# Kernel tuning notes

Hardware: AMD Instinct MI355X
Metric: run time of the kernel (lower is better)

Reference implementation:

```python
import jax, jax.numpy as jnp
import numpy as np

DIM = 256

def _feat(x):
    # ELU(x) + 1 feature map (positive features for linear attention)
    return jax.nn.elu(x) + 1.0

def setup_inputs() -> dict:
    key = jax.random.key(0)
    ks = jax.random.split(key, 9)
    B, L, D = 8, 4096, DIM
    s = 1.0 / np.sqrt(D)
    return {
        'q': jax.random.normal(ks[0], (B, L, D), jnp.float32),
        'k': jax.random.normal(ks[1], (B, L, D), jnp.float32),
        'v': jax.random.normal(ks[2], (B, L, D), jnp.float32),
        'Wq': jax.random.normal(ks[3], (D, D), jnp.float32) * s,
        'bq': jnp.zeros((D,), jnp.float32),
        'Wk': jax.random.normal(ks[4], (D, D), jnp.float32) * s,
        'bk': jnp.zeros((D,), jnp.float32),
        'Wv': jax.random.normal(ks[5], (D, D), jnp.float32) * s,
        'bv': jnp.zeros((D,), jnp.float32),
    }

def reference(q, k, v, Wq, bq, Wk, bk, Wv, bv):
    Q = _feat(q @ Wq + bq)              # [B,L,D]
    K = _feat(k @ Wk + bk)              # [B,L,D]
    V = v @ Wv + bv                     # [B,L,D]
    kv = jnp.einsum('bld,blh->bdh', K, V)          # [B,D,D] summary
    z = jnp.einsum('bld,bd->bl', Q, K.sum(axis=1)) + 1e-6  # [B,L]
    out = jnp.einsum('bld,bdh->blh', Q, kv)        # [B,L,D]
    return out / z[..., None]
```

## Files before the change

kernel.cpp:

```cpp
#include <hip/hip_runtime.h>
#include <hip/hip_bf16.h>

#define DIM 256
#define BATCH 8
#define SEQ 4096
#define MTOT (BATCH*SEQ)
#define LDP 40

typedef __attribute__((ext_vector_type(8))) short bf16x8;
typedef __attribute__((ext_vector_type(4))) float f32x4;
typedef __attribute__((ext_vector_type(8))) unsigned short u16x8;
typedef __attribute__((ext_vector_type(4))) unsigned short u16x4;

__device__ inline unsigned short f2b(float f){
  unsigned int u = __float_as_uint(f);
  u = u + 0x7FFFu + ((u >> 16) & 1u);
  return (unsigned short)(u >> 16);
}
__device__ inline float b2f(unsigned short h){
  return __uint_as_float(((unsigned int)h) << 16);
}

template<bool F32SRC>
__device__ inline void stage_tile(const void* src, int ld, int tid, unsigned short* lds){
  int row = tid >> 1, kh = tid & 1;
  unsigned short tmp[16];
  if constexpr (F32SRC) {
    const float* p = (const float*)src + (long)row*ld + kh*16;
    #pragma unroll
    for (int j = 0; j < 16; j += 4){
      f32x4 f = *(const f32x4*)(p + j);
      tmp[j+0] = f2b(f[0]); tmp[j+1] = f2b(f[1]);
      tmp[j+2] = f2b(f[2]); tmp[j+3] = f2b(f[3]);
    }
  } else {
    const unsigned short* p = (const unsigned short*)src + (long)row*ld + kh*16;
    *(u16x8*)&tmp[0] = *(const u16x8*)p;
    *(u16x8*)&tmp[8] = *(const u16x8*)(p + 8);
  }
  unsigned short* d = lds + row*LDP + kh*16;
  *(u16x8*)d       = *(u16x8*)&tmp[0];
  *(u16x8*)(d + 8) = *(u16x8*)&tmp[8];
}

__device__ inline void mma_step(const unsigned short* lA, const unsigned short* lB,
                                int lane, int wr, int wc, f32x4 acc[4][4]){
  int r0 = lane & 15, ko = (lane >> 4) * 8;
  bf16x8 af[4], bf[4];
  #pragma unroll
  for (int m = 0; m < 4; m++) af[m] = *(const bf16x8*)&lA[(wr*64 + m*16 + r0)*LDP + ko];
  #pragma unroll
  for (int n = 0; n < 4; n++) bf[n] = *(const bf16x8*)&lB[(wc*64 + n*16 + r0)*LDP + ko];
  #pragma unroll
  for (int m = 0; m < 4; m++)
    #pragma unroll
    for (int n = 0; n < 4; n++)
      acc[m][n] = __builtin_amdgcn_mfma_f32_16x16x32_bf16(af[m], bf[n], acc[m][n], 0, 0, 0);
}

__global__ __launch_bounds__(256) void prep_wt(const float* __restrict__ Wq, const float* __restrict__ Wk,
                                               const float* __restrict__ Wv, unsigned short* __restrict__ Wt){
  int i = blockIdx.x*256 + threadIdx.x;
  int s = i >> 16, r = i & 65535, n = r & 255, kk = r >> 8;
  const float* W = (s == 0) ? Wq : ((s == 1) ? Wk : Wv);
  Wt[s*65536 + n*256 + kk] = f2b(W[kk*256 + n]);
}

__global__ __launch_bounds__(256) void proj_all_ker(const float* __restrict__ qin, const float* __restrict__ kin,
                                                    const float* __restrict__ vin,
                                                    const unsigned short* __restrict__ Wt,
                                                    const float* __restrict__ bqp, const float* __restrict__ bkp,
                                                    const float* __restrict__ bvp,
                                                    unsigned short* __restrict__ Qo,
                                                    unsigned short* __restrict__ Kt, unsigned short* __restrict__ Vt,
                                                    float* __restrict__ ksum){
  __shared__ unsigned short lA[128*LDP], lB[128*LDP];
  int lt = blockIdx.x, dt = blockIdx.y;
  int bz = blockIdx.z, sel = bz % 3, b = bz / 3;
  int tid = threadIdx.x, lane = tid & 63, w = tid >> 6, wr = w >> 1, wc = w & 1;

  const float* X = (sel == 0 ? kin : (sel == 1 ? vin : qin)) + ((long)b*SEQ + (long)lt*128)*DIM;
  const unsigned short* Wb = Wt + ((sel + 1) % 3)*DIM*DIM + dt*128*DIM;
  const float* bias = (sel == 0 ? bkp : (sel == 1 ? bvp : bqp));

  f32x4 acc[4][4] = {};
  for (int ks = 0; ks < DIM/32; ks++){
    __syncthreads();
    if (sel == 2){
      stage_tile<true >(X  + ks*32, DIM, tid, lA);
      stage_tile<false>(Wb + ks*32, DIM, tid, lB);
    } else {
      stage_tile<false>(Wb + ks*32, DIM, tid, lA);
      stage_tile<true >(X  + ks*32, DIM, tid, lB);
    }
    __syncthreads();
    mma_step(lA, lB, lane, wr, wc, acc);
  }
  int r0 = lane & 15, rg = lane >> 4;

  if (sel == 2){
    #pragma unroll
    for (int n = 0; n < 4; n++){
      int col = dt*128 + wc*64 + n*16 + r0;
      float bv = bias[col];
      #pragma unroll
      for (int m = 0; m < 4; m++){
        #pragma unroll
        for (int r = 0; r < 4; r++){
          long row = (long)b*SEQ + lt*128 + wr*64 + m*16 + rg*4 + r;
          float vv = acc[m][n][r] + bv;
          vv = vv > 0.f ? vv + 1.f : expf(vv);
          Qo[row*DIM + col] = f2b(vv);
        }
      }
    }
    return;
  }

  unsigned short* Yt = (sel == 1 ? Vt : Kt) + (long)b*DIM*SEQ;
  float sums[4][4];
  #pragma unroll
  for (int m = 0; m < 4; m++) for (int r = 0; r < 4; r++) sums[m][r] = 0.f;
  #pragma unroll
  for (int m = 0; m < 4; m++){
    #pragma unroll
    for (int r = 0; r < 4; r++){
      int row = dt*128 + wr*64 + m*16 + rg*4 + r;
      float bvv = bias[row];
      #pragma unroll
      for (int n = 0; n < 4; n++){
        int col = lt*128 + wc*64 + n*16 + r0;
        float vv = acc[m][n][r] + bvv;
        if (sel == 0) vv = vv > 0.f ? vv + 1.f : expf(vv);
        Yt[(long)row*SEQ + col] = f2b(vv);
        sums[m][r] += vv;
      }
    }
  }
  if (sel == 0){
    #pragma unroll
    for (int m = 0; m < 4; m++){
      #pragma unroll
      for (int r = 0; r < 4; r++){
        float s = sums[m][r];
        s += __shfl_xor(s, 1); s += __shfl_xor(s, 2);
        s += __shfl_xor(s, 4); s += __shfl_xor(s, 8);
        if (r0 == 0){
          int row = dt*128 + wr*64 + m*16 + rg*4 + r;
          atomicAdd(&ksum[b*DIM + row], s);
        }
      }
    }
  }
}

__global__ __launch_bounds__(256) void kv_ker(const unsigned short* __restrict__ Vt, const unsigned short* __restrict__ Kt,
                                              float* __restrict__ kvf){
  __shared__ unsigned short lA[128*LDP], lB[128*LDP];
  int qd = blockIdx.x, mt = qd >> 1, nt = qd & 1;
  int ksp = blockIdx.y, b = blockIdx.z;
  int tid = threadIdx.x, lane = tid & 63, w = tid >> 6, wr = w >> 1, wc = w & 1;
  const unsigned short* A  = Vt + (long)b*DIM*SEQ + (long)mt*128*SEQ + ksp*256;
  const unsigned short* Bb = Kt + (long)b*DIM*SEQ + (long)nt*128*SEQ + ksp*256;
  f32x4 acc[4][4] = {};
  for (int ks = 0; ks < 8; ks++){
    __syncthreads();
    stage_tile<false>(A  + ks*32, SEQ, tid, lA);
    stage_tile<false>(Bb + ks*32, SEQ, tid, lB);
    __syncthreads();
    mma_step(lA, lB, lane, wr, wc, acc);
  }
  int r0 = lane & 15, rg = lane >> 4;
  float* base = kvf + (long)b*DIM*DIM;
  #pragma unroll
  for (int m = 0; m < 4; m++)
    #pragma unroll
    for (int n = 0; n < 4; n++)
      #pragma unroll
      for (int r = 0; r < 4; r++){
        int row = mt*128 + wr*64 + m*16 + rg*4 + r;
        int col = nt*128 + wc*64 + n*16 + r0;
        atomicAdd(&base[row*DIM + col], acc[m][n][r]);
      }
}

__global__ __launch_bounds__(256) void zker(const unsigned short* __restrict__ Q, const float* __restrict__ ksum,
                                            float* __restrict__ z){
  int g = blockIdx.x*4 + (threadIdx.x >> 6);
  int lane = threadIdx.x & 63;
  int b = g >> 12;
  u16x4 qv = *(const u16x4*)(Q + (long)g*DIM + lane*4);
  const float* kp = ksum + b*DIM + lane*4;
  float s = b2f(qv[0])*kp[0] + b2f(qv[1])*kp[1] + b2f(qv[2])*kp[2] + b2f(qv[3])*kp[3];
  #pragma unroll
  for (int o = 1; o < 64; o <<= 1) s += __shfl_xor(s, o);
  if (lane == 0) z[g] = s + 1e-6f;
}

__global__ __launch_bounds__(256) void out_ker(const unsigned short* __restrict__ Q, const float* __restrict__ kvf,
                                               const float* __restrict__ z, float* __restrict__ out){
  __shared__ unsigned short lA[128*LDP], lB[128*LDP];
  int lt = blockIdx.x, ht = blockIdx.y, b = blockIdx.z;
  int tid = threadIdx.x, lane = tid & 63, w = tid >> 6, wr = w >> 1, wc = w & 1;
  const unsigned short* A = Q + ((long)b*SEQ + (long)lt*128)*DIM;
  const float* Bb = kvf + b*DIM*DIM + ht*128*DIM;
  f32x4 acc[4][4] = {};
  for (int ks = 0; ks < DIM/32; ks++){
    __syncthreads();
    stage_tile<false>(A  + ks*32, DIM, tid, lA);
    stage_tile<true >(Bb + ks*32, DIM, tid, lB);
    __syncthreads();
    mma_step(lA, lB, lane, wr, wc, acc);
  }
  int r0 = lane & 15, rg = lane >> 4;
  #pragma unroll
  for (int m = 0; m < 4; m++){
    #pragma unroll
    for (int r = 0; r < 4; r++){
      long g = (long)b*SEQ + lt*128 + wr*64 + m*16 + rg*4 + r;
      float inv = 1.0f / z[g];
      #pragma unroll
      for (int n = 0; n < 4; n++){
        int col = ht*128 + wc*64 + n*16 + r0;
        out[g*DIM + col] = acc[m][n][r] * inv;
      }
    }
  }
}

extern "C" void kernel_launch(void* const* d_in, const int* in_sizes, int n_in,
                              void* d_out, int out_size, void* d_ws, size_t ws_size,
                              hipStream_t stream){
  const float* q  = (const float*)d_in[0];
  const float* k  = (const float*)d_in[1];
  const float* v  = (const float*)d_in[2];
  const float* Wq = (const float*)d_in[3];
  const float* bq = (const float*)d_in[4];
  const float* Wk = (const float*)d_in[5];
  const float* bk = (const float*)d_in[6];
  const float* Wv = (const float*)d_in[7];
  const float* bv = (const float*)d_in[8];
  float* out = (float*)d_out;

  char* ws = (char*)d_ws;
  size_t off = 0;
  auto alloc = [&](size_t bytes){ void* p = ws + off; off += (bytes + 255) & ~(size_t)255; return p; };
  unsigned short* Q   = (unsigned short*)alloc((size_t)MTOT*DIM*2);
  unsigned short* Kt  = (unsigned short*)alloc((size_t)BATCH*DIM*SEQ*2);
  unsigned short* Vt  = (unsigned short*)alloc((size_t)BATCH*DIM*SEQ*2);
  unsigned short* Wt  = (unsigned short*)alloc((size_t)3*DIM*DIM*2);
  float*          kvf = (float*)alloc((size_t)BATCH*DIM*DIM*4);
  float*          ksum= (float*)alloc((size_t)BATCH*DIM*4);
  float*          zb  = (float*)alloc((size_t)MTOT*4);

  hipMemsetAsync(kvf, 0, (size_t)BATCH*DIM*DIM*4 + (size_t)BATCH*DIM*4, stream);

  hipLaunchKernelGGL(prep_wt,     dim3(768),     dim3(256), 0, stream, Wq, Wk, Wv, Wt);
  hipLaunchKernelGGL(proj_all_ker,dim3(32,2,24), dim3(256), 0, stream, q, k, v, Wt, bq, bk, bv, Q, Kt, Vt, ksum);
  hipLaunchKernelGGL(kv_ker,      dim3(4,16,8),  dim3(256), 0, stream, Vt, Kt, kvf);
  hipLaunchKernelGGL(zker,        dim3(8192),    dim3(256), 0, stream, Q, ksum, zb);
  hipLaunchKernelGGL(out_ker,     dim3(32,2,8),  dim3(256), 0, stream, Q, kvf, zb, out);
}
```

Before: 254.0 us.

## Stage 128-wide K halves in swizzled LDS with register prefetch; split-K KV without atomics

The GEMM mainloop now stages 128-element K halves into XOR-swizzled LDS, and loads the second half into registers while the first half is being multiplied. This cuts the number of barriers per tile and is meant to avoid bank conflicts. The KV reduction now writes per-split partials, which a new reduce kernel sums and converts to bf16. This replaces float atomics and the memset, and lets out_ker read bf16 kv directly. In exchange it uses much more LDS (64KB per block), carries a heavy register load of prefetch buffers that may lower occupancy, and adds an extra kernel launch and partial-buffer traffic.

Result: faster. 235.5 us (-7.3%).

```diff
diff --git a/kernel.cpp b/kernel.cpp
--- a/kernel.cpp
+++ b/kernel.cpp
@@ -5,7 +5,7 @@
 #define BATCH 8
 #define SEQ 4096
 #define MTOT (BATCH*SEQ)
-#define LDP 40
+#define NSPLIT 8
 
 typedef __attribute__((ext_vector_type(8))) short bf16x8;
 typedef __attribute__((ext_vector_type(4))) float f32x4;
@@ -21,41 +21,90 @@
   return __uint_as_float(((unsigned int)h) << 16);
 }
 
-template<bool F32SRC>
-__device__ inline void stage_tile(const void* src, int ld, int tid, unsigned short* lds){
-  int row = tid >> 1, kh = tid & 1;
-  unsigned short tmp[16];
-  if constexpr (F32SRC) {
-    const float* p = (const float*)src + (long)row*ld + kh*16;
-    #pragma unroll
-    for (int j = 0; j < 16; j += 4){
-      f32x4 f = *(const f32x4*)(p + j);
-      tmp[j+0] = f2b(f[0]); tmp[j+1] = f2b(f[1]);
-      tmp[j+2] = f2b(f[2]); tmp[j+3] = f2b(f[3]);
-    }
+
+template<bool F32>
+__device__ inline void load_half(const void* src, int ld, int h, int tid,
+                                 f32x4* vf, u16x8* vh){
+  int row = tid >> 1, c0 = h*128 + (tid & 1)*64;
+  if constexpr (F32){
+    const float* p = (const float*)src + (long)row*ld + c0;
+    #pragma unroll
+    for (int j = 0; j < 16; j++) vf[j] = *(const f32x4*)(p + 4*j);
   } else {
-    const unsigned short* p = (const unsigned short*)src + (long)row*ld + kh*16;
-    *(u16x8*)&tmp[0] = *(const u16x8*)p;
-    *(u16x8*)&tmp[8] = *(const u16x8*)(p + 8);
-  }
-  unsigned short* d = lds + row*LDP + kh*16;
-  *(u16x8*)d       = *(u16x8*)&tmp[0];
-  *(u16x8*)(d + 8) = *(u16x8*)&tmp[8];
-}
-
-__device__ inline void mma_step(const unsigned short* lA, const unsigned short* lB,
+    const unsigned short* p = (const unsigned short*)src + (long)row*ld + c0;
+    #pragma unroll
+    for (int j = 0; j < 8; j++) vh[j] = *(const u16x8*)(p + 8*j);
+  }
+}
+
+template<bool F32>
+__device__ inline void write_half(const f32x4* vf, const u16x8* vh, int tid,
+                                  unsigned short* lds){
+  unsigned short tmp[64];
+  if constexpr (F32){
+    #pragma unroll
+    for (int j = 0; j < 16; j++){
+      f32x4 f = vf[j];
+      tmp[4*j+0] = f2b(f[0]); tmp[4*j+1] = f2b(f[1]);
+      tmp[4*j+2] = f2b(f[2]); tmp[4*j+3] = f2b(f[3]);
+    }
+  } else {
+    #pragma unroll
+    for (int j = 0; j < 8; j++) *(u16x8*)&tmp[8*j] = vh[j];
+  }
+  int row = tid >> 1, sw = (row & 7) << 4;
+  char* rb = (char*)lds + row*256 + (tid & 1)*128;
+  #pragma unroll
+  for (int j = 0; j < 8; j++)
+    *(u16x8*)(rb + ((j*16) ^ sw)) = *(const u16x8*)&tmp[8*j];
+}
+
+__device__ inline void mma_half(const unsigned short* lA, const unsigned short* lB,
                                 int lane, int wr, int wc, f32x4 acc[4][4]){
-  int r0 = lane & 15, ko = (lane >> 4) * 8;
-  bf16x8 af[4], bf[4];
-  #pragma unroll
-  for (int m = 0; m < 4; m++) af[m] = *(const bf16x8*)&lA[(wr*64 + m*16 + r0)*LDP + ko];
-  #pragma unroll
-  for (int n = 0; n < 4; n++) bf[n] = *(const bf16x8*)&lB[(wc*64 + n*16 + r0)*LDP + ko];
-  #pragma unroll
-  for (int m = 0; m < 4; m++)
-    #pragma unroll
-    for (int n = 0; n < 4; n++)
-      acc[m][n] = __builtin_amdgcn_mfma_f32_16x16x32_bf16(af[m], bf[n], acc[m][n], 0, 0, 0);
+  int r0 = lane & 15, kg16 = (lane >> 4) * 16;
+  #pragma unroll
+  for (int ksub = 0; ksub < 4; ksub++){
+    int kb = ksub*64 + kg16;
+    bf16x8 af[4], bf[4];
+    #pragma unroll
+    for (int m = 0; m < 4; m++){
+      int row = wr*64 + m*16 + r0;
+      af[m] = *(const bf16x8*)((const char*)lA + row*256 + (kb ^ ((row & 7) << 4)));
+    }
+    #pragma unroll
+    for (int n = 0; n < 4; n++){
+      int row = wc*64 + n*16 + r0;
+      bf[n] = *(const bf16x8*)((const char*)lB + row*256 + (kb ^ ((row & 7) << 4)));
+    }
+    #pragma unroll
+    for (int m = 0; m < 4; m++)
+      #pragma unroll
+      for (int n = 0; n < 4; n++)
+        acc[m][n] = __builtin_amdgcn_mfma_f32_16x16x32_bf16(af[m], bf[n], acc[m][n], 0, 0, 0);
+  }
+}
+
+template<bool AF32, bool BF32>
+__device__ inline void gemm256(const void* A, int lda, const void* B, int ldb,
+                               int tid, int lane, int wr, int wc,
+                               unsigned short* lA, unsigned short* lB,
+                               f32x4 acc[4][4]){
+  f32x4 a0f[16], a1f[16], b0f[16], b1f[16];
+  u16x8 a0h[8], a1h[8], b0h[8], b1h[8];
+  load_half<AF32>(A, lda, 0, tid, a0f, a0h);
+  load_half<BF32>(B, ldb, 0, tid, b0f, b0h);
+  __syncthreads();
+  write_half<AF32>(a0f, a0h, tid, lA);
+  write_half<BF32>(b0f, b0h, tid, lB);
+  load_half<AF32>(A, lda, 1, tid, a1f, a1h);
+  load_half<BF32>(B, ldb, 1, tid, b1f, b1h);
+  __syncthreads();
+  mma_half(lA, lB, lane, wr, wc, acc);
+  __syncthreads();
+  write_half<AF32>(a1f, a1h, tid, lA);
+  write_half<BF32>(b1f, b1h, tid, lB);
+  __syncthreads();
+  mma_half(lA, lB, lane, wr, wc, acc);
 }
 
 __global__ __launch_bounds__(256) void prep_wt(const float* __restrict__ Wq, const float* __restrict__ Wk,
@@ -74,7 +123,7 @@
                                                     unsigned short* __restrict__ Qo,
                                                     unsigned short* __restrict__ Kt, unsigned short* __restrict__ Vt,
                                                     float* __restrict__ ksum){
-  __shared__ unsigned short lA[128*LDP], lB[128*LDP];
+  __shared__ unsigned short lA[128*128], lB[128*128];
   int lt = blockIdx.x, dt = blockIdx.y;
   int bz = blockIdx.z, sel = bz % 3, b = bz / 3;
   int tid = threadIdx.x, lane = tid & 63, w = tid >> 6, wr = w >> 1, wc = w & 1;
@@ -84,18 +133,9 @@
   const float* bias = (sel == 0 ? bkp : (sel == 1 ? bvp : bqp));
 
   f32x4 acc[4][4] = {};
-  for (int ks = 0; ks < DIM/32; ks++){
-    __syncthreads();
-    if (sel == 2){
-      stage_tile<true >(X  + ks*32, DIM, tid, lA);
-      stage_tile<false>(Wb + ks*32, DIM, tid, lB);
-    } else {
-      stage_tile<false>(Wb + ks*32, DIM, tid, lA);
-      stage_tile<true >(X  + ks*32, DIM, tid, lB);
-    }
-    __syncthreads();
-    mma_step(lA, lB, lane, wr, wc, acc);
-  }
+  if (sel == 2) gemm256<true , false>(X , DIM, Wb, DIM, tid, lane, wr, wc, lA, lB, acc);
+  else          gemm256<false, true >(Wb, DIM, X , DIM, tid, lane, wr, wc, lA, lB, acc);
+
   int r0 = lane & 15, rg = lane >> 4;
 
   if (sel == 2){
@@ -104,7 +144,7 @@
       int col = dt*128 + wc*64 + n*16 + r0;
       float bv = bias[col];
       #pragma unroll
-      for (int m = 0; m < 4; m++){
+      for (int m = 0; m < 4; m++)
         #pragma unroll
         for (int r = 0; r < 4; r++){
           long row = (long)b*SEQ + lt*128 + wr*64 + m*16 + rg*4 + r;
@@ -112,7 +152,6 @@
           vv = vv > 0.f ? vv + 1.f : expf(vv);
           Qo[row*DIM + col] = f2b(vv);
         }
-      }
     }
     return;
   }
@@ -122,7 +161,7 @@
   #pragma unroll
   for (int m = 0; m < 4; m++) for (int r = 0; r < 4; r++) sums[m][r] = 0.f;
   #pragma unroll
-  for (int m = 0; m < 4; m++){
+  for (int m = 0; m < 4; m++)
     #pragma unroll
     for (int r = 0; r < 4; r++){
       int row = dt*128 + wr*64 + m*16 + rg*4 + r;
@@ -136,10 +175,9 @@
         sums[m][r] += vv;
       }
     }
-  }
   if (sel == 0){
     #pragma unroll
-    for (int m = 0; m < 4; m++){
+    for (int m = 0; m < 4; m++)
       #pragma unroll
       for (int r = 0; r < 4; r++){
         float s = sums[m][r];
@@ -150,28 +188,22 @@
           atomicAdd(&ksum[b*DIM + row], s);
         }
       }
-    }
   }
 }
 
 __global__ __launch_bounds__(256) void kv_ker(const unsigned short* __restrict__ Vt, const unsigned short* __restrict__ Kt,
-                                              float* __restrict__ kvf){
-  __shared__ unsigned short lA[128*LDP], lB[128*LDP];
+                                              float* __restrict__ kvp){
+  __shared__ unsigned short lA[128*128], lB[128*128];
   int qd = blockIdx.x, mt = qd >> 1, nt = qd & 1;
   int ksp = blockIdx.y, b = blockIdx.z;
   int tid = threadIdx.x, lane = tid & 63, w = tid >> 6, wr = w >> 1, wc = w & 1;
-  const unsigned short* A  = Vt + (long)b*DIM*SEQ + (long)mt*128*SEQ + ksp*256;
-  const unsigned short* Bb = Kt + (long)b*DIM*SEQ + (long)nt*128*SEQ + ksp*256;
+  const unsigned short* A = Vt + (long)b*DIM*SEQ + (long)mt*128*SEQ + ksp*512;
+  const unsigned short* B = Kt + (long)b*DIM*SEQ + (long)nt*128*SEQ + ksp*512;
   f32x4 acc[4][4] = {};
-  for (int ks = 0; ks < 8; ks++){
-    __syncthreads();
-    stage_tile<false>(A  + ks*32, SEQ, tid, lA);
-    stage_tile<false>(Bb + ks*32, SEQ, tid, lB);
-    __syncthreads();
-    mma_step(lA, lB, lane, wr, wc, acc);
-  }
+  gemm256<false,false>(A      , SEQ, B      , SEQ, tid, lane, wr, wc, lA, lB, acc);
+  gemm256<false,false>(A + 256, SEQ, B + 256, SEQ, tid, lane, wr, wc, lA, lB, acc);
   int r0 = lane & 15, rg = lane >> 4;
-  float* base = kvf + (long)b*DIM*DIM;
+  float* base = kvp + (long)(ksp*BATCH + b)*DIM*DIM;
   #pragma unroll
   for (int m = 0; m < 4; m++)
     #pragma unroll
@@ -180,8 +212,17 @@
       for (int r = 0; r < 4; r++){
         int row = mt*128 + wr*64 + m*16 + rg*4 + r;
         int col = nt*128 + wc*64 + n*16 + r0;
-        atomicAdd(&base[row*DIM + col], acc[m][n][r]);
-      }
+        base[row*DIM + col] = acc[m][n][r];
+      }
+}
+
+__global__ __launch_bounds__(256) void kv_reduce(const float* __restrict__ kvp, unsigned short* __restrict__ kvb){
+  int i = blockIdx.x*256 + threadIdx.x;
+  int b = i >> 16, e = i & 65535;
+  float s = 0.f;
+  #pragma unroll
+  for (int sp = 0; sp < NSPLIT; sp++) s += kvp[(long)(sp*BATCH + b)*65536 + e];
+  kvb[i] = f2b(s);
 }
 
 __global__ __launch_bounds__(256) void zker(const unsigned short* __restrict__ Q, const float* __restrict__ ksum,
@@ -197,24 +238,18 @@
   if (lane == 0) z[g] = s + 1e-6f;
 }
 
-__global__ __launch_bounds__(256) void out_ker(const unsigned short* __restrict__ Q, const float* __restrict__ kvf,
+__global__ __launch_bounds__(256) void out_ker(const unsigned short* __restrict__ Q, const unsigned short* __restrict__ kvb,
                                                const float* __restrict__ z, float* __restrict__ out){
-  __shared__ unsigned short lA[128*LDP], lB[128*LDP];
+  __shared__ unsigned short lA[128*128], lB[128*128];
   int lt = blockIdx.x, ht = blockIdx.y, b = blockIdx.z;
   int tid = threadIdx.x, lane = tid & 63, w = tid >> 6, wr = w >> 1, wc = w & 1;
   const unsigned short* A = Q + ((long)b*SEQ + (long)lt*128)*DIM;
-  const float* Bb = kvf + b*DIM*DIM + ht*128*DIM;
+  const unsigned short* B = kvb + b*DIM*DIM + ht*128*DIM;
   f32x4 acc[4][4] = {};
-  for (int ks = 0; ks < DIM/32; ks++){
-    __syncthreads();
-    stage_tile<false>(A  + ks*32, DIM, tid, lA);
-    stage_tile<true >(Bb + ks*32, DIM, tid, lB);
-    __syncthreads();
-    mma_step(lA, lB, lane, wr, wc, acc);
-  }
+  gemm256<false,false>(A, DIM, B, DIM, tid, lane, wr, wc, lA, lB, acc);
   int r0 = lane & 15, rg = lane >> 4;
   #pragma unroll
-  for (int m = 0; m < 4; m++){
+  for (int m = 0; m < 4; m++)
     #pragma unroll
     for (int r = 0; r < 4; r++){
       long g = (long)b*SEQ + lt*128 + wr*64 + m*16 + rg*4 + r;
@@ -225,7 +260,6 @@
         out[g*DIM + col] = acc[m][n][r] * inv;
       }
     }
-  }
 }
 
 extern "C" void kernel_launch(void* const* d_in, const int* in_sizes, int n_in,
@@ -249,15 +283,17 @@
   unsigned short* Kt  = (unsigned short*)alloc((size_t)BATCH*DIM*SEQ*2);
   unsigned short* Vt  = (unsigned short*)alloc((size_t)BATCH*DIM*SEQ*2);
   unsigned short* Wt  = (unsigned short*)alloc((size_t)3*DIM*DIM*2);
-  float*          kvf = (float*)alloc((size_t)BATCH*DIM*DIM*4);
+  float*          kvp = (float*)alloc((size_t)NSPLIT*BATCH*DIM*DIM*4);
+  unsigned short* kvb = (unsigned short*)alloc((size_t)BATCH*DIM*DIM*2);
   float*          ksum= (float*)alloc((size_t)BATCH*DIM*4);
   float*          zb  = (float*)alloc((size_t)MTOT*4);
 
-  hipMemsetAsync(kvf, 0, (size_t)BATCH*DIM*DIM*4 + (size_t)BATCH*DIM*4, stream);
-
-  hipLaunchKernelGGL(prep_wt,     dim3(768),     dim3(256), 0, stream, Wq, Wk, Wv, Wt);
-  hipLaunchKernelGGL(proj_all_ker,dim3(32,2,24), dim3(256), 0, stream, q, k, v, Wt, bq, bk, bv, Q, Kt, Vt, ksum);
-  hipLaunchKernelGGL(kv_ker,      dim3(4,16,8),  dim3(256), 0, stream, Vt, Kt, kvf);
-  hipLaunchKernelGGL(zker,        dim3(8192),    dim3(256), 0, stream, Q, ksum, zb);
-  hipLaunchKernelGGL(out_ker,     dim3(32,2,8),  dim3(256), 0, stream, Q, kvf, zb, out);
-}
+  hipMemsetAsync(ksum, 0, (size_t)BATCH*DIM*4, stream);
+
+  hipLaunchKernelGGL(prep_wt,     dim3(768),        dim3(256), 0, stream, Wq, Wk, Wv, Wt);
+  hipLaunchKernelGGL(proj_all_ker,dim3(32,2,24),    dim3(256), 0, stream, q, k, v, Wt, bq, bk, bv, Q, Kt, Vt, ksum);
+  hipLaunchKernelGGL(kv_ker,      dim3(4,NSPLIT,8), dim3(256), 0, stream, Vt, Kt, kvp);
+  hipLaunchKernelGGL(kv_reduce,   dim3(2048),       dim3(256), 0, stream, kvp, kvb);
+  hipLaunchKernelGGL(zker,        dim3(8192),       dim3(256), 0, stream, Q, ksum, zb);
+  hipLaunchKernelGGL(out_ker,     dim3(32,2,8),     dim3(256), 0, stream, Q, kvb, zb, out);
+}
```
